# Optimization experiments

Measured on AMD Instinct MI355X. Metric: run time of the kernel, lower is better.

Reference implementation:

```python
import jax, jax.numpy as jnp
import numpy as np

# MX microscaling spec: block_size=32 shared power-of-2 scale, int8 elements (MXINT8),
# vector (SIMD) ops rounded to bfloat16 as in microxcaling's simd_* / vec_* ops.
BLOCK = 32
BITS = 8  # int8 element format: grid step 2^(shared_exp - (BITS-2)), range [-2^(BITS-1), 2^(BITS-1)-1]


def bf16_round(x):
    # bfloat=16 rounding used by simd_split / simd_add / vec ops
    return x.astype(jnp.bfloat16).astype(jnp.float32)


def mx_quant(x):
    """MXINT8 fake-quant along last (contraction) axis with block-shared exponent.
    Straight-through estimator for gradients."""
    s = x.shape
    xb = x.reshape(s[:-1] + (s[-1] // BLOCK, BLOCK))
    amax = jnp.max(jnp.abs(xb), axis=-1, keepdims=True)
    shared_exp = jnp.floor(jnp.log2(jnp.where(amax > 0, amax, 1.0)))
    scale = jnp.exp2(shared_exp - (BITS - 2))
    q = jnp.clip(jnp.round(xb / scale), -(2.0 ** (BITS - 1)), 2.0 ** (BITS - 1) - 1) * scale
    q = jnp.where(amax > 0, q, 0.0).reshape(s)
    return x + jax.lax.stop_gradient(q - x)


def mx_linear(x, W, b):
    # quantize activations and weights to MX blocks along K, fp32 accumulate, bf16 bias-add
    y = jnp.einsum('btk,ok->bto', mx_quant(x), mx_quant(W))
    return bf16_round(y + b)


def mx_layernorm(x, w, b, eps=1e-5):
    mu = jnp.mean(x, axis=-1, keepdims=True)
    var = jnp.mean(jnp.square(x - mu), axis=-1, keepdims=True)
    return bf16_round((x - mu) * jax.lax.rsqrt(var + eps) * w + b)


def mx_gelu(x):
    # tanh-approx gelu as in microxcaling, bf16-rounded output
    c = jnp.float32(0.7978845608028654)  # sqrt(2/pi)
    return bf16_round(0.5 * x * (1.0 + jnp.tanh(c * (x + 0.044715 * x * x * x))))


def setup_inputs() -> dict:
    key = jax.random.key(0)
    ks = jax.random.split(key, 5)
    B, S, H = 2, 2048, 2048
    inputs = jax.random.normal(ks[0], (B, S, H), dtype=jnp.float32)
    ln_w = jnp.ones((H,), dtype=jnp.float32)
    ln_b = jnp.zeros((H,), dtype=jnp.float32)
    W1 = jax.random.normal(ks[1], (4 * H, H), dtype=jnp.float32) * (1.0 / np.sqrt(H))
    b1 = jnp.zeros((4 * H,), dtype=jnp.float32)
    W2 = jax.random.normal(ks[2], (H, 4 * H), dtype=jnp.float32) * (1.0 / np.sqrt(4 * H))
    b2 = jnp.zeros((H,), dtype=jnp.float32)
    return {"inputs": inputs, "ln_w": ln_w, "ln_b": ln_b, "W1": W1, "b1": b1, "W2": W2, "b2": b2}


def reference(inputs, ln_w, ln_b, W1, b1, W2, b2):
    # simd_split: bf16-rounded copies for MLP branch and residual branch
    x = bf16_round(inputs)
    residual = bf16_round(inputs)
    h = mx_layernorm(x, ln_w, ln_b)
    h = mx_linear(h, W1, b1)          # [B,S,4H]
    h = mx_gelu(h)
    h = mx_linear(h, W2, b2)          # [B,S,H]
    return bf16_round(residual + h)    # simd_add
```

## Files before the change

kernel.cpp:

```cpp
#include <hip/hip_runtime.h>

#define DEVI __device__ __forceinline__

typedef __bf16 bf16x8 __attribute__((ext_vector_type(8)));
typedef float f32x4 __attribute__((ext_vector_type(4)));

DEVI unsigned short f2bf(float f) {
  unsigned u = __float_as_uint(f);
  u = (u + 0x7FFFu + ((u >> 16) & 1u)) >> 16;
  return (unsigned short)u;
}
DEVI float bf2f(unsigned short h) { return __uint_as_float(((unsigned)h) << 16); }
DEVI float bf16r(float f) { return bf2f(f2bf(f)); }

DEVI void mx_scales(float amax, float& scale, float& inv) {
  unsigned eb = __float_as_uint(amax) & 0x7f800000u;
  scale = __uint_as_float(eb - (6u << 23));
  inv   = __uint_as_float((260u << 23) - eb);
}

DEVI unsigned short quantv(float v, float scale, float inv) {
  float qv = rintf(v * inv);
  qv = fminf(fmaxf(qv, -128.f), 127.f);
  return f2bf(qv * scale);
}

DEVI void quant8(const float* h, float amax, unsigned short* q) {
  if (amax > 0.f) {
    float scale, inv;
    mx_scales(amax, scale, inv);
#pragma unroll
    for (int k = 0; k < 8; ++k) q[k] = quantv(h[k], scale, inv);
  } else {
#pragma unroll
    for (int k = 0; k < 8; ++k) q[k] = 0;
  }
}

template <int N>
DEVI float qmax_step(float x) {
  int y = __builtin_amdgcn_update_dpp(0, __float_as_int(x), 0x120 | N, 0xF, 0xF, true);
  return fmaxf(x, __int_as_float(y));
}
DEVI float quad_row_max(float x) {
  x = qmax_step<1>(x);
  x = qmax_step<2>(x);
  x = qmax_step<4>(x);
  x = qmax_step<8>(x);
  return x;
}

DEVI void gl2lds16(const void* g, void* l) {
  __builtin_amdgcn_global_load_lds(
      (__attribute__((address_space(1))) void*)const_cast<void*>(g),
      (__attribute__((address_space(3))) void*)l, 16, 0, 0);
}

DEVI uint4 pack8(const unsigned short* q) {
  uint4 o;
  o.x = (unsigned)q[0] | ((unsigned)q[1] << 16);
  o.y = (unsigned)q[2] | ((unsigned)q[3] << 16);
  o.z = (unsigned)q[4] | ((unsigned)q[5] << 16);
  o.w = (unsigned)q[6] | ((unsigned)q[7] << 16);
  return o;
}

__global__ __launch_bounds__(256) void prep_k(const float* __restrict__ W1,
                                              const float* __restrict__ W2,
                                              const float* __restrict__ X,
                                              const float* __restrict__ lw,
                                              const float* __restrict__ lb,
                                              unsigned short* __restrict__ qW1,
                                              unsigned short* __restrict__ qW2,
                                              unsigned short* __restrict__ a1) {
  __shared__ float red[4];
  const int bid = blockIdx.x;
  const int t = threadIdx.x;
  if (bid < 16384) {
    const float* src = (bid < 8192) ? W1 : W2;
    unsigned short* dst = (bid < 8192) ? qW1 : qW2;
    size_t idx = (size_t)(bid & 8191) * 256 + t;
    float4 v0 = ((const float4*)src)[idx * 2];
    float4 v1 = ((const float4*)src)[idx * 2 + 1];
    float h[8] = {v0.x, v0.y, v0.z, v0.w, v1.x, v1.y, v1.z, v1.w};
    float amax = 0.f;
#pragma unroll
    for (int k = 0; k < 8; ++k) amax = fmaxf(amax, fabsf(h[k]));
    amax = fmaxf(amax, __shfl_xor(amax, 1));
    amax = fmaxf(amax, __shfl_xor(amax, 2));
    unsigned short q[8];
    quant8(h, amax, q);
    ((uint4*)dst)[idx] = pack8(q);
  } else {
    const int H = 2048;
    const int row = bid - 16384;
    const int lane = t & 63, wave = t >> 6;
    const float* xr = X + (size_t)row * H;
    float4 v0 = ((const float4*)xr)[2 * t];
    float4 v1 = ((const float4*)xr)[2 * t + 1];
    float x[8] = {bf16r(v0.x), bf16r(v0.y), bf16r(v0.z), bf16r(v0.w),
                  bf16r(v1.x), bf16r(v1.y), bf16r(v1.z), bf16r(v1.w)};
    float s = 0.f;
#pragma unroll
    for (int k = 0; k < 8; ++k) s += x[k];
#pragma unroll
    for (int o = 32; o; o >>= 1) s += __shfl_xor(s, o);
    if (lane == 0) red[wave] = s;
    __syncthreads();
    float mu = (red[0] + red[1] + red[2] + red[3]) * (1.0f / H);
    __syncthreads();
    float v = 0.f;
#pragma unroll
    for (int k = 0; k < 8; ++k) { float d = x[k] - mu; v += d * d; }
#pragma unroll
    for (int o = 32; o; o >>= 1) v += __shfl_xor(v, o);
    if (lane == 0) red[wave] = v;
    __syncthreads();
    float var = (red[0] + red[1] + red[2] + red[3]) * (1.0f / H);
    float rstd = 1.0f / sqrtf(var + 1e-5f);
    float h[8];
    float amax = 0.f;
#pragma unroll
    for (int k = 0; k < 8; ++k) {
      int col = t * 8 + k;
      h[k] = bf16r((x[k] - mu) * rstd * lw[col] + lb[col]);
      amax = fmaxf(amax, fabsf(h[k]));
    }
    amax = fmaxf(amax, __shfl_xor(amax, 1));
    amax = fmaxf(amax, __shfl_xor(amax, 2));
    unsigned short q[8];
    quant8(h, amax, q);
    ((uint4*)(a1 + (size_t)row * H))[t] = pack8(q);
  }
}

template <int MODE>
__global__ __launch_bounds__(256) void gemm_mx(const unsigned short* __restrict__ A,
                                               const unsigned short* __restrict__ B,
                                               int M, int N, int K,
                                               const float* __restrict__ bias,
                                               const float* __restrict__ resid,
                                               void* __restrict__ outp) {
  __shared__ unsigned short As[128 * 64];
  __shared__ unsigned short Bs[128 * 64];

  const int tid = threadIdx.x;
  const int lane = tid & 63;
  const int wave = tid >> 6;
  const int wr = (wave >> 1) * 64;
  const int wc = (wave & 1) * 64;
  const int lr = lane & 15;
  const int quad = lane >> 4;

  const int m0 = blockIdx.y * 128;
  const int n0 = blockIdx.x * 128;

  size_t aoff[4], boff[4];
  int lbase[4];
#pragma unroll
  for (int j = 0; j < 4; ++j) {
    int n = j * 256 + tid;
    int r = n >> 3, c = (n & 7) ^ (r & 7);
    aoff[j] = (size_t)(m0 + r) * K + (size_t)c * 8;
    boff[j] = (size_t)(n0 + r) * K + (size_t)c * 8;
    lbase[j] = (j * 256 + (tid & ~63)) * 8;
  }

  f32x4 acc[4][4];
#pragma unroll
  for (int i = 0; i < 4; ++i)
#pragma unroll
    for (int j = 0; j < 4; ++j) acc[i][j] = (f32x4){0.f, 0.f, 0.f, 0.f};

  for (int k0 = 0; k0 < K; k0 += 64) {
#pragma unroll
    for (int j = 0; j < 4; ++j) gl2lds16(A + aoff[j] + k0, As + lbase[j]);
#pragma unroll
    for (int j = 0; j < 4; ++j) gl2lds16(B + boff[j] + k0, Bs + lbase[j]);
    __syncthreads();
#pragma unroll
    for (int s = 0; s < 2; ++s) {
      bf16x8 af[4], bfr[4];
#pragma unroll
      for (int i = 0; i < 4; ++i) {
        int row = wr + i * 16 + lr;
        int ch = (s * 4 + quad) ^ (row & 7);
        af[i] = *(const bf16x8*)(As + row * 64 + ch * 8);
      }
#pragma unroll
      for (int j = 0; j < 4; ++j) {
        int row = wc + j * 16 + lr;
        int ch = (s * 4 + quad) ^ (row & 7);
        bfr[j] = *(const bf16x8*)(Bs + row * 64 + ch * 8);
      }
#pragma unroll
      for (int i = 0; i < 4; ++i)
#pragma unroll
        for (int j = 0; j < 4; ++j)
          acc[i][j] = __builtin_amdgcn_mfma_f32_16x16x32_bf16(af[i], bfr[j], acc[i][j], 0, 0, 0);
    }
    __syncthreads();
  }

  if (MODE == 1) {
#pragma unroll
    for (int i = 0; i < 4; ++i) {
#pragma unroll
      for (int r = 0; r < 4; ++r) {
        const int gm = m0 + wr + i * 16 + quad * 4 + r;
        float g[4];
#pragma unroll
        for (int j = 0; j < 4; ++j) {
          float t = bf16r(acc[i][j][r] + bias[n0 + wc + j * 16 + lr]);
          float u = 0.7978845608028654f * (t + 0.044715f * t * t * t);
          g[j] = bf16r(0.5f * t * (1.0f + tanhf(u)));
        }
        float a = quad_row_max(fmaxf(fabsf(g[0]), fabsf(g[1])));
        float b = quad_row_max(fmaxf(fabsf(g[2]), fabsf(g[3])));
        unsigned short q[4];
        if (a > 0.f) {
          float sc, iv; mx_scales(a, sc, iv);
          q[0] = quantv(g[0], sc, iv); q[1] = quantv(g[1], sc, iv);
        } else { q[0] = q[1] = 0; }
        if (b > 0.f) {
          float sc, iv; mx_scales(b, sc, iv);
          q[2] = quantv(g[2], sc, iv); q[3] = quantv(g[3], sc, iv);
        } else { q[2] = q[3] = 0; }
        unsigned short* orow = (unsigned short*)outp + (size_t)gm * N + n0 + wc + lr;
#pragma unroll
        for (int j = 0; j < 4; ++j) orow[j * 16] = q[j];
      }
    }
  } else {
#pragma unroll
    for (int i = 0; i < 4; ++i) {
#pragma unroll
      for (int j = 0; j < 4; ++j) {
#pragma unroll
        for (int r = 0; r < 4; ++r) {
          int gm = m0 + wr + i * 16 + quad * 4 + r;
          int gn = n0 + wc + j * 16 + lr;
          float h = bf16r(acc[i][j][r] + bias[gn]);
          float rr = bf16r(resid[(size_t)gm * N + gn]);
          ((float*)outp)[(size_t)gm * N + gn] = bf16r(rr + h);
        }
      }
    }
  }
  (void)M;
}

extern "C" void kernel_launch(void* const* d_in, const int* in_sizes, int n_in,
                              void* d_out, int out_size, void* d_ws, size_t ws_size,
                              hipStream_t stream) {
  const float* inputs = (const float*)d_in[0];
  const float* ln_w   = (const float*)d_in[1];
  const float* ln_b   = (const float*)d_in[2];
  const float* W1     = (const float*)d_in[3];
  const float* b1     = (const float*)d_in[4];
  const float* W2     = (const float*)d_in[5];
  const float* b2     = (const float*)d_in[6];
  float* out = (float*)d_out;
  char* ws = (char*)d_ws;
  (void)in_sizes; (void)n_in; (void)out_size; (void)ws_size;

  unsigned short* qW1  = (unsigned short*)(ws);
  unsigned short* qW2  = (unsigned short*)(ws + (size_t)33554432);
  unsigned short* a1   = (unsigned short*)(ws + (size_t)67108864);
  unsigned short* act2 = (unsigned short*)(ws + (size_t)83886080);

  const int M = 4096;

  prep_k<<<20480, 256, 0, stream>>>(W1, W2, inputs, ln_w, ln_b, qW1, qW2, a1);

  gemm_mx<1><<<dim3(8192 / 128, M / 128), 256, 0, stream>>>(
      a1, qW1, M, 8192, 2048, b1, nullptr, (void*)act2);

  gemm_mx<2><<<dim3(2048 / 128, M / 128), 256, 0, stream>>>(
      act2, qW2, M, 2048, 8192, b2, inputs, (void*)out);
}
```

Baseline: 507.6 us.

## Triple-buffer GEMM LDS tiles with async prefetch and 128x256 block tiles

```diff
diff --git a/kernel.cpp b/kernel.cpp
--- a/kernel.cpp
+++ b/kernel.cpp
@@ -135,36 +135,38 @@
 }
 
 template <int MODE>
-__global__ __launch_bounds__(256) void gemm_mx(const unsigned short* __restrict__ A,
-                                               const unsigned short* __restrict__ B,
-                                               int M, int N, int K,
-                                               const float* __restrict__ bias,
-                                               const float* __restrict__ resid,
-                                               void* __restrict__ outp) {
-  __shared__ unsigned short As[128 * 64];
-  __shared__ unsigned short Bs[128 * 64];
+__global__ __launch_bounds__(512, 2) void gemm_mx(const unsigned short* __restrict__ A,
+                                                  const unsigned short* __restrict__ B,
+                                                  int M, int N, int K,
+                                                  const float* __restrict__ bias,
+                                                  const float* __restrict__ resid,
+                                                  void* __restrict__ outp) {
+  __shared__ __align__(16) unsigned short As[3][2][128 * 32];
+  __shared__ __align__(16) unsigned short Bs[3][2][256 * 32];
 
   const int tid = threadIdx.x;
   const int lane = tid & 63;
   const int wave = tid >> 6;
-  const int wr = (wave >> 1) * 64;
-  const int wc = (wave & 1) * 64;
   const int lr = lane & 15;
   const int quad = lane >> 4;
+  const int wr = (wave >> 2) * 64;
+  const int wc = (wave & 3) * 64;
 
   const int m0 = blockIdx.y * 128;
-  const int n0 = blockIdx.x * 128;
-
-  size_t aoff[4], boff[4];
-  int lbase[4];
-#pragma unroll
-  for (int j = 0; j < 4; ++j) {
-    int n = j * 256 + tid;
-    int r = n >> 3, c = (n & 7) ^ (r & 7);
-    aoff[j] = (size_t)(m0 + r) * K + (size_t)c * 8;
-    boff[j] = (size_t)(n0 + r) * K + (size_t)c * 8;
-    lbase[j] = (j * 256 + (tid & ~63)) * 8;
-  }
+  const int n0 = blockIdx.x * 256;
+
+  const int xsw = (quad ^ (lr & 3)) << 3;
+  const int lro = (wr + lr) * 32 + xsw;
+  const int lco = (wc + lr) * 32 + xsw;
+
+  const int sr = tid >> 2;
+  const int sc = ((tid & 3) ^ (sr & 3)) << 3;
+  const size_t aoff  = (size_t)(m0 + sr) * K + sc;
+  const size_t boff0 = (size_t)(n0 + sr) * K + sc;
+  const size_t boff1 = (size_t)(n0 + 128 + sr) * K + sc;
+  const int lbase = (tid & ~63) * 8;
+
+  const int NT = K >> 6;
 
   f32x4 acc[4][4];
 #pragma unroll
@@ -172,34 +174,54 @@
 #pragma unroll
     for (int j = 0; j < 4; ++j) acc[i][j] = (f32x4){0.f, 0.f, 0.f, 0.f};
 
-  for (int k0 = 0; k0 < K; k0 += 64) {
-#pragma unroll
-    for (int j = 0; j < 4; ++j) gl2lds16(A + aoff[j] + k0, As + lbase[j]);
-#pragma unroll
-    for (int j = 0; j < 4; ++j) gl2lds16(B + boff[j] + k0, Bs + lbase[j]);
-    __syncthreads();
+#pragma unroll
+  for (int pt = 0; pt < 2; ++pt)
+#pragma unroll
+    for (int s = 0; s < 2; ++s) {
+      const size_t kadd = (size_t)pt * 64 + s * 32;
+      gl2lds16(A + aoff + kadd, &As[pt][s][lbase]);
+      gl2lds16(B + boff0 + kadd, &Bs[pt][s][lbase]);
+      gl2lds16(B + boff1 + kadd, &Bs[pt][s][4096 + lbase]);
+    }
+  asm volatile("s_waitcnt vmcnt(6)" ::: "memory");
+  __builtin_amdgcn_s_barrier();
+
+  int buf = 0;
+  for (int t = 0; t < NT; ++t) {
+    int nbuf = buf + 2; if (nbuf >= 3) nbuf -= 3;
+    const bool pf = (t + 2) < NT;
 #pragma unroll
     for (int s = 0; s < 2; ++s) {
       bf16x8 af[4], bfr[4];
-#pragma unroll
-      for (int i = 0; i < 4; ++i) {
-        int row = wr + i * 16 + lr;
-        int ch = (s * 4 + quad) ^ (row & 7);
-        af[i] = *(const bf16x8*)(As + row * 64 + ch * 8);
+      const unsigned short* Ap = &As[buf][s][0];
+      const unsigned short* Bp = &Bs[buf][s][0];
+#pragma unroll
+      for (int i = 0; i < 4; ++i) af[i] = *(const bf16x8*)(Ap + lro + i * 512);
+#pragma unroll
+      for (int j = 0; j < 4; ++j) bfr[j] = *(const bf16x8*)(Bp + lco + j * 512);
+      if (pf) {
+        const size_t kadd = (size_t)(t + 2) * 64 + s * 32;
+        gl2lds16(A + aoff + kadd, &As[nbuf][s][lbase]);
+        gl2lds16(B + boff0 + kadd, &Bs[nbuf][s][lbase]);
+        gl2lds16(B + boff1 + kadd, &Bs[nbuf][s][4096 + lbase]);
       }
-#pragma unroll
-      for (int j = 0; j < 4; ++j) {
-        int row = wc + j * 16 + lr;
-        int ch = (s * 4 + quad) ^ (row & 7);
-        bfr[j] = *(const bf16x8*)(Bs + row * 64 + ch * 8);
-      }
+      __builtin_amdgcn_s_barrier();
+      asm volatile("s_waitcnt lgkmcnt(0)" ::: "memory");
+      __builtin_amdgcn_sched_barrier(0);
+      __builtin_amdgcn_s_setprio(1);
 #pragma unroll
       for (int i = 0; i < 4; ++i)
 #pragma unroll
         for (int j = 0; j < 4; ++j)
           acc[i][j] = __builtin_amdgcn_mfma_f32_16x16x32_bf16(af[i], bfr[j], acc[i][j], 0, 0, 0);
-    }
-    __syncthreads();
+      __builtin_amdgcn_s_setprio(0);
+      if (s == 1) {
+        if (pf) asm volatile("s_waitcnt vmcnt(6)" ::: "memory");
+        else    asm volatile("s_waitcnt vmcnt(0)" ::: "memory");
+      }
+      __builtin_amdgcn_s_barrier();
+    }
+    if (++buf == 3) buf = 0;
   }
 
   if (MODE == 1) {
@@ -211,20 +233,20 @@
         float g[4];
 #pragma unroll
         for (int j = 0; j < 4; ++j) {
-          float t = bf16r(acc[i][j][r] + bias[n0 + wc + j * 16 + lr]);
-          float u = 0.7978845608028654f * (t + 0.044715f * t * t * t);
-          g[j] = bf16r(0.5f * t * (1.0f + tanhf(u)));
+          float tt = bf16r(acc[i][j][r] + bias[n0 + wc + j * 16 + lr]);
+          float u = 0.7978845608028654f * (tt + 0.044715f * tt * tt * tt);
+          g[j] = bf16r(0.5f * tt * (1.0f + tanhf(u)));
         }
         float a = quad_row_max(fmaxf(fabsf(g[0]), fabsf(g[1])));
         float b = quad_row_max(fmaxf(fabsf(g[2]), fabsf(g[3])));
         unsigned short q[4];
         if (a > 0.f) {
-          float sc, iv; mx_scales(a, sc, iv);
-          q[0] = quantv(g[0], sc, iv); q[1] = quantv(g[1], sc, iv);
+          float sc2, iv; mx_scales(a, sc2, iv);
+          q[0] = quantv(g[0], sc2, iv); q[1] = quantv(g[1], sc2, iv);
         } else { q[0] = q[1] = 0; }
         if (b > 0.f) {
-          float sc, iv; mx_scales(b, sc, iv);
-          q[2] = quantv(g[2], sc, iv); q[3] = quantv(g[3], sc, iv);
+          float sc2, iv; mx_scales(b, sc2, iv);
+          q[2] = quantv(g[2], sc2, iv); q[3] = quantv(g[3], sc2, iv);
         } else { q[2] = q[3] = 0; }
         unsigned short* orow = (unsigned short*)outp + (size_t)gm * N + n0 + wc + lr;
 #pragma unroll
@@ -273,9 +295,9 @@
 
   prep_k<<<20480, 256, 0, stream>>>(W1, W2, inputs, ln_w, ln_b, qW1, qW2, a1);
 
-  gemm_mx<1><<<dim3(8192 / 128, M / 128), 256, 0, stream>>>(
+  gemm_mx<1><<<dim3(8192 / 256, M / 128), 512, 0, stream>>>(
       a1, qW1, M, 8192, 2048, b1, nullptr, (void*)act2);
 
-  gemm_mx<2><<<dim3(2048 / 128, M / 128), 256, 0, stream>>>(
+  gemm_mx<2><<<dim3(2048 / 256, M / 128), 512, 0, stream>>>(
       act2, qW2, M, 2048, 8192, b2, inputs, (void*)out);
 }
```

After: 558.4 us. 10.0% more time.

## Rewrite both GEMMs with multi-stage LDS pipelining, larger tiles and swizzled block order

Applied to the files above, without the earlier changes.

```diff
diff --git a/kernel.cpp b/kernel.cpp
--- a/kernel.cpp
+++ b/kernel.cpp
@@ -4,6 +4,9 @@
 
 typedef __bf16 bf16x8 __attribute__((ext_vector_type(8)));
 typedef float f32x4 __attribute__((ext_vector_type(4)));
+
+#define WAIT_VM(n) asm volatile("s_waitcnt vmcnt(" #n ")" ::: "memory")
+#define WAIT_LGKM(n) asm volatile("s_waitcnt lgkmcnt(" #n ")" ::: "memory")
 
 DEVI unsigned short f2bf(float f) {
   unsigned u = __float_as_uint(f);
@@ -134,37 +137,166 @@
   }
 }
 
-template <int MODE>
-__global__ __launch_bounds__(256) void gemm_mx(const unsigned short* __restrict__ A,
-                                               const unsigned short* __restrict__ B,
-                                               int M, int N, int K,
-                                               const float* __restrict__ bias,
-                                               const float* __restrict__ resid,
-                                               void* __restrict__ outp) {
-  __shared__ unsigned short As[128 * 64];
-  __shared__ unsigned short Bs[128 * 64];
+__global__ __launch_bounds__(512, 2) void gemm1_k(const unsigned short* __restrict__ A,
+                                                  const unsigned short* __restrict__ B,
+                                                  const float* __restrict__ bias,
+                                                  unsigned short* __restrict__ outp) {
+  constexpr int K = 2048, N = 8192, NT = K / 32;
+  __shared__ __align__(16) unsigned short As[4 * 8192];
+  __shared__ __align__(16) unsigned short Bs[4 * 8192];
 
   const int tid = threadIdx.x;
   const int lane = tid & 63;
-  const int wave = tid >> 6;
-  const int wr = (wave >> 1) * 64;
-  const int wc = (wave & 1) * 64;
   const int lr = lane & 15;
   const int quad = lane >> 4;
-
-  const int m0 = blockIdx.y * 128;
-  const int n0 = blockIdx.x * 128;
-
-  size_t aoff[4], boff[4];
-  int lbase[4];
-#pragma unroll
-  for (int j = 0; j < 4; ++j) {
-    int n = j * 256 + tid;
-    int r = n >> 3, c = (n & 7) ^ (r & 7);
-    aoff[j] = (size_t)(m0 + r) * K + (size_t)c * 8;
-    boff[j] = (size_t)(n0 + r) * K + (size_t)c * 8;
-    lbase[j] = (j * 256 + (tid & ~63)) * 8;
-  }
+  const int wave = tid >> 6;
+  const int wm = wave >> 2;
+  const int wn = wave & 3;
+
+  int lin = blockIdx.y * 32 + blockIdx.x;
+  lin = (lin & 7) * 64 + (lin >> 3);
+  const int m0 = (lin >> 5) * 256;
+  const int n0 = (lin & 31) * 256;
+
+  const int chq = quad ^ ((lr >> 1) & 3);
+  const int aro = (wm * 128 + lr) * 32 + chq * 8;
+  const int bro = (wn * 64 + lr) * 32 + chq * 8;
+
+  const int srow = tid >> 2;
+  const int sch = (tid & 3) ^ ((tid >> 3) & 3);
+  const size_t aoff = (size_t)(m0 + srow) * K + sch * 8;
+  const size_t boff = (size_t)(n0 + srow) * K + sch * 8;
+  const int lb = (tid & ~63) * 8;
+
+  f32x4 acc[8][4];
+#pragma unroll
+  for (int i = 0; i < 8; ++i)
+#pragma unroll
+    for (int j = 0; j < 4; ++j) acc[i][j] = (f32x4){0.f, 0.f, 0.f, 0.f};
+
+  bf16x8 af0[4], af1[4], bA[4], bB[4];
+
+#define G1_STAGE_A(T) { int bf_ = (T) & 3;                                         \
+    gl2lds16(A + aoff + (size_t)(T) * 32, As + bf_ * 8192 + lb);                   \
+    gl2lds16(A + aoff + (size_t)128 * K + (size_t)(T) * 32, As + bf_ * 8192 + 4096 + lb); }
+#define G1_STAGE_B(T) { int bf_ = (T) & 3;                                         \
+    gl2lds16(B + boff + (size_t)(T) * 32, Bs + bf_ * 8192 + lb);                   \
+    gl2lds16(B + boff + (size_t)128 * K + (size_t)(T) * 32, Bs + bf_ * 8192 + 4096 + lb); }
+
+#pragma unroll
+  for (int pt = 0; pt < 3; ++pt) { G1_STAGE_A(pt); G1_STAGE_B(pt); }
+  WAIT_VM(8);
+  __builtin_amdgcn_s_barrier();
+#pragma unroll
+  for (int i = 0; i < 4; ++i) af0[i] = *(const bf16x8*)(As + aro + i * 512);
+#pragma unroll
+  for (int j = 0; j < 4; ++j) bA[j] = *(const bf16x8*)(Bs + bro + j * 512);
+
+#define G1_TILE(T, BC, BN_) {                                                      \
+    const unsigned short* Ab_ = As + ((T) & 3) * 8192;                             \
+    const bool pf3 = (T) + 3 < NT, pf2 = (T) + 2 < NT, pf1 = (T) + 1 < NT;         \
+                      \
+    if (pf3) G1_STAGE_A((T) + 3);                                                  \
+    _Pragma("unroll")                                                              \
+    for (int i = 0; i < 4; ++i) af1[i] = *(const bf16x8*)(Ab_ + aro + 2048 + i * 512); \
+    if (pf3) { WAIT_VM(6); } else if (pf2) { WAIT_VM(4); } else { WAIT_VM(0); }    \
+    WAIT_LGKM(4);                                                                  \
+    __builtin_amdgcn_sched_barrier(0);                                             \
+    __builtin_amdgcn_s_setprio(1);                                                 \
+    _Pragma("unroll")                                                              \
+    for (int i = 0; i < 4; ++i)                                                    \
+      _Pragma("unroll")                                                            \
+      for (int j = 0; j < 4; ++j)                                                  \
+        acc[i][j] = __builtin_amdgcn_mfma_f32_16x16x32_bf16(af0[i], BC[j], acc[i][j], 0, 0, 0); \
+    __builtin_amdgcn_s_setprio(0);                                                 \
+    __builtin_amdgcn_s_barrier();                                                  \
+           \
+    if (pf3) G1_STAGE_B((T) + 3);                                                  \
+    if (pf1) {                                                                     \
+      const unsigned short* An_ = As + (((T) + 1) & 3) * 8192;                     \
+      const unsigned short* Bn_ = Bs + (((T) + 1) & 3) * 8192;                     \
+      _Pragma("unroll")                                                            \
+      for (int i = 0; i < 4; ++i) af0[i] = *(const bf16x8*)(An_ + aro + i * 512);  \
+      _Pragma("unroll")                                                            \
+      for (int j = 0; j < 4; ++j) BN_[j] = *(const bf16x8*)(Bn_ + bro + j * 512);  \
+      WAIT_LGKM(8);                                                                \
+    } else { WAIT_LGKM(0); }                                                       \
+    __builtin_amdgcn_sched_barrier(0);                                             \
+    __builtin_amdgcn_s_setprio(1);                                                 \
+    _Pragma("unroll")                                                              \
+    for (int i = 0; i < 4; ++i)                                                    \
+      _Pragma("unroll")                                                            \
+      for (int j = 0; j < 4; ++j)                                                  \
+        acc[4 + i][j] = __builtin_amdgcn_mfma_f32_16x16x32_bf16(af1[i], BC[j], acc[4 + i][j], 0, 0, 0); \
+    __builtin_amdgcn_s_setprio(0);                                                 \
+    __builtin_amdgcn_s_barrier(); }
+
+  for (int t = 0; t < NT; t += 2) {
+    G1_TILE(t, bA, bB);
+    G1_TILE(t + 1, bB, bA);
+  }
+
+#pragma unroll
+  for (int i = 0; i < 8; ++i) {
+#pragma unroll
+    for (int r = 0; r < 4; ++r) {
+      const int gm = m0 + wm * 128 + i * 16 + quad * 4 + r;
+      float g[4];
+#pragma unroll
+      for (int j = 0; j < 4; ++j) {
+        float tt = bf16r(acc[i][j][r] + bias[n0 + wn * 64 + j * 16 + lr]);
+        float u = 0.7978845608028654f * (tt + 0.044715f * tt * tt * tt);
+        g[j] = bf16r(0.5f * tt * (1.0f + tanhf(u)));
+      }
+      float a = quad_row_max(fmaxf(fabsf(g[0]), fabsf(g[1])));
+      float b = quad_row_max(fmaxf(fabsf(g[2]), fabsf(g[3])));
+      unsigned short q[4];
+      if (a > 0.f) {
+        float sc2, iv; mx_scales(a, sc2, iv);
+        q[0] = quantv(g[0], sc2, iv); q[1] = quantv(g[1], sc2, iv);
+      } else { q[0] = q[1] = 0; }
+      if (b > 0.f) {
+        float sc2, iv; mx_scales(b, sc2, iv);
+        q[2] = quantv(g[2], sc2, iv); q[3] = quantv(g[3], sc2, iv);
+      } else { q[2] = q[3] = 0; }
+      unsigned short* orow = outp + (size_t)gm * N + n0 + wn * 64 + lr;
+#pragma unroll
+      for (int j = 0; j < 4; ++j) orow[j * 16] = q[j];
+    }
+  }
+}
+
+__global__ __launch_bounds__(512, 2) void gemm2_k(const unsigned short* __restrict__ A,
+                                                  const unsigned short* __restrict__ B,
+                                                  const float* __restrict__ bias,
+                                                  const float* __restrict__ resid,
+                                                  float* __restrict__ outp) {
+  constexpr int K = 8192, N = 2048, NT = K / 32;
+  __shared__ __align__(16) unsigned short As[5 * 4096];
+  __shared__ __align__(16) unsigned short Bs[5 * 8192];
+
+  const int tid = threadIdx.x;
+  const int lane = tid & 63;
+  const int lr = lane & 15;
+  const int quad = lane >> 4;
+  const int wave = tid >> 6;
+  const int wm = wave >> 2;
+  const int wn = wave & 3;
+
+  int lin = blockIdx.y * 8 + blockIdx.x;
+  lin = (lin & 7) * 32 + (lin >> 3);
+  const int m0 = (lin >> 3) * 128;
+  const int n0 = (lin & 7) * 256;
+
+  const int chq = quad ^ ((lr >> 1) & 3);
+  const int aro = (wm * 64 + lr) * 32 + chq * 8;
+  const int bro = (wn * 64 + lr) * 32 + chq * 8;
+
+  const int srow = tid >> 2;
+  const int sch = (tid & 3) ^ ((tid >> 3) & 3);
+  const size_t aoff = (size_t)(m0 + srow) * K + sch * 8;
+  const size_t boff = (size_t)(n0 + srow) * K + sch * 8;
+  const int lb = (tid & ~63) * 8;
 
   f32x4 acc[4][4];
 #pragma unroll
@@ -172,82 +304,64 @@
 #pragma unroll
     for (int j = 0; j < 4; ++j) acc[i][j] = (f32x4){0.f, 0.f, 0.f, 0.f};
 
-  for (int k0 = 0; k0 < K; k0 += 64) {
-#pragma unroll
-    for (int j = 0; j < 4; ++j) gl2lds16(A + aoff[j] + k0, As + lbase[j]);
-#pragma unroll
-    for (int j = 0; j < 4; ++j) gl2lds16(B + boff[j] + k0, Bs + lbase[j]);
-    __syncthreads();
-#pragma unroll
-    for (int s = 0; s < 2; ++s) {
-      bf16x8 af[4], bfr[4];
-#pragma unroll
-      for (int i = 0; i < 4; ++i) {
-        int row = wr + i * 16 + lr;
-        int ch = (s * 4 + quad) ^ (row & 7);
-        af[i] = *(const bf16x8*)(As + row * 64 + ch * 8);
-      }
-#pragma unroll
-      for (int j = 0; j < 4; ++j) {
-        int row = wc + j * 16 + lr;
-        int ch = (s * 4 + quad) ^ (row & 7);
-        bfr[j] = *(const bf16x8*)(Bs + row * 64 + ch * 8);
-      }
-#pragma unroll
-      for (int i = 0; i < 4; ++i)
-#pragma unroll
-        for (int j = 0; j < 4; ++j)
-          acc[i][j] = __builtin_amdgcn_mfma_f32_16x16x32_bf16(af[i], bfr[j], acc[i][j], 0, 0, 0);
-    }
-    __syncthreads();
-  }
-
-  if (MODE == 1) {
-#pragma unroll
-    for (int i = 0; i < 4; ++i) {
+  bf16x8 afX[4], bX[4], afY[4], bY[4];
+
+#define G2_STAGE(T) { int bf_ = (T) % 5;                                           \
+    gl2lds16(A + aoff + (size_t)(T) * 32, As + bf_ * 4096 + lb);                   \
+    gl2lds16(B + boff + (size_t)(T) * 32, Bs + bf_ * 8192 + lb);                   \
+    gl2lds16(B + boff + (size_t)128 * K + (size_t)(T) * 32, Bs + bf_ * 8192 + 4096 + lb); }
+
+#pragma unroll
+  for (int pt = 0; pt < 4; ++pt) G2_STAGE(pt);
+  WAIT_VM(6);
+  __builtin_amdgcn_s_barrier();
+#pragma unroll
+  for (int i = 0; i < 4; ++i) afX[i] = *(const bf16x8*)(As + aro + i * 512);
+#pragma unroll
+  for (int j = 0; j < 4; ++j) bX[j] = *(const bf16x8*)(Bs + bro + j * 512);
+
+#define G2_TILE(T, AC, BC, AN, BN_) {                                              \
+    const bool pf4 = (T) + 4 < NT, pf3 = (T) + 3 < NT, pf1 = (T) + 1 < NT;         \
+    if (pf1) {                                                                     \
+      const unsigned short* An_ = As + (((T) + 1) % 5) * 4096;                     \
+      const unsigned short* Bn_ = Bs + (((T) + 1) % 5) * 8192;                     \
+      _Pragma("unroll")                                                            \
+      for (int i = 0; i < 4; ++i) AN[i] = *(const bf16x8*)(An_ + aro + i * 512);   \
+      _Pragma("unroll")                                                            \
+      for (int j = 0; j < 4; ++j) BN_[j] = *(const bf16x8*)(Bn_ + bro + j * 512);  \
+    }                                                                              \
+    if (pf4) G2_STAGE((T) + 4);                                                    \
+    if (pf4) { WAIT_VM(6); } else if (pf3) { WAIT_VM(3); } else { WAIT_VM(0); }    \
+    if (pf1) { WAIT_LGKM(8); } else { WAIT_LGKM(0); }                              \
+    __builtin_amdgcn_sched_barrier(0);                                             \
+    __builtin_amdgcn_s_setprio(1);                                                 \
+    _Pragma("unroll")                                                              \
+    for (int i = 0; i < 4; ++i)                                                    \
+      _Pragma("unroll")                                                            \
+      for (int j = 0; j < 4; ++j)                                                  \
+        acc[i][j] = __builtin_amdgcn_mfma_f32_16x16x32_bf16(AC[i], BC[j], acc[i][j], 0, 0, 0); \
+    __builtin_amdgcn_s_setprio(0);                                                 \
+    __builtin_amdgcn_s_barrier(); }
+
+  for (int t = 0; t < NT; t += 2) {
+    G2_TILE(t, afX, bX, afY, bY);
+    G2_TILE(t + 1, afY, bY, afX, bX);
+  }
+
+#pragma unroll
+  for (int i = 0; i < 4; ++i) {
+#pragma unroll
+    for (int j = 0; j < 4; ++j) {
 #pragma unroll
       for (int r = 0; r < 4; ++r) {
-        const int gm = m0 + wr + i * 16 + quad * 4 + r;
-        float g[4];
-#pragma unroll
-        for (int j = 0; j < 4; ++j) {
-          float t = bf16r(acc[i][j][r] + bias[n0 + wc + j * 16 + lr]);
-          float u = 0.7978845608028654f * (t + 0.044715f * t * t * t);
-          g[j] = bf16r(0.5f * t * (1.0f + tanhf(u)));
-        }
-        float a = quad_row_max(fmaxf(fabsf(g[0]), fabsf(g[1])));
-        float b = quad_row_max(fmaxf(fabsf(g[2]), fabsf(g[3])));
-        unsigned short q[4];
-        if (a > 0.f) {
-          float sc, iv; mx_scales(a, sc, iv);
-          q[0] = quantv(g[0], sc, iv); q[1] = quantv(g[1], sc, iv);
-        } else { q[0] = q[1] = 0; }
-        if (b > 0.f) {
-          float sc, iv; mx_scales(b, sc, iv);
-          q[2] = quantv(g[2], sc, iv); q[3] = quantv(g[3], sc, iv);
-        } else { q[2] = q[3] = 0; }
-        unsigned short* orow = (unsigned short*)outp + (size_t)gm * N + n0 + wc + lr;
-#pragma unroll
-        for (int j = 0; j < 4; ++j) orow[j * 16] = q[j];
+        int gm = m0 + wm * 64 + i * 16 + quad * 4 + r;
+        int gn = n0 + wn * 64 + j * 16 + lr;
+        float h = bf16r(acc[i][j][r] + bias[gn]);
+        float rr = bf16r(resid[(size_t)gm * N + gn]);
+        outp[(size_t)gm * N + gn] = bf16r(rr + h);
       }
     }
-  } else {
-#pragma unroll
-    for (int i = 0; i < 4; ++i) {
-#pragma unroll
-      for (int j = 0; j < 4; ++j) {
-#pragma unroll
-        for (int r = 0; r < 4; ++r) {
-          int gm = m0 + wr + i * 16 + quad * 4 + r;
-          int gn = n0 + wc + j * 16 + lr;
-          float h = bf16r(acc[i][j][r] + bias[gn]);
-          float rr = bf16r(resid[(size_t)gm * N + gn]);
-          ((float*)outp)[(size_t)gm * N + gn] = bf16r(rr + h);
-        }
-      }
-    }
-  }
-  (void)M;
+  }
 }
 
 extern "C" void kernel_launch(void* const* d_in, const int* in_sizes, int n_in,
@@ -269,13 +383,9 @@
   unsigned short* a1   = (unsigned short*)(ws + (size_t)67108864);
   unsigned short* act2 = (unsigned short*)(ws + (size_t)83886080);
 
-  const int M = 4096;
-
   prep_k<<<20480, 256, 0, stream>>>(W1, W2, inputs, ln_w, ln_b, qW1, qW2, a1);
 
-  gemm_mx<1><<<dim3(8192 / 128, M / 128), 256, 0, stream>>>(
-      a1, qW1, M, 8192, 2048, b1, nullptr, (void*)act2);
-
-  gemm_mx<2><<<dim3(2048 / 128, M / 128), 256, 0, stream>>>(
-      act2, qW2, M, 2048, 8192, b2, inputs, (void*)out);
-}
+  gemm1_k<<<dim3(8192 / 256, 4096 / 256), 512, 0, stream>>>(a1, qW1, b1, act2);
+
+  gemm2_k<<<dim3(2048 / 256, 4096 / 128), 512, 0, stream>>>(act2, qW2, b2, inputs, out);
+}
```

After: 538.5 us. 6.1% more time.

## Load B fragments directly from global into registers with double-buffered prefetch

Applied to the files above, without the earlier changes.

```diff
diff --git a/kernel.cpp b/kernel.cpp
--- a/kernel.cpp
+++ b/kernel.cpp
@@ -142,7 +142,6 @@
                                                const float* __restrict__ resid,
                                                void* __restrict__ outp) {
   __shared__ unsigned short As[128 * 64];
-  __shared__ unsigned short Bs[128 * 64];
 
   const int tid = threadIdx.x;
   const int lane = tid & 63;
@@ -155,52 +154,76 @@
   const int m0 = blockIdx.y * 128;
   const int n0 = blockIdx.x * 128;
 
-  size_t aoff[4], boff[4];
+  size_t aoff[4];
   int lbase[4];
 #pragma unroll
   for (int j = 0; j < 4; ++j) {
     int n = j * 256 + tid;
     int r = n >> 3, c = (n & 7) ^ (r & 7);
     aoff[j] = (size_t)(m0 + r) * K + (size_t)c * 8;
-    boff[j] = (size_t)(n0 + r) * K + (size_t)c * 8;
     lbase[j] = (j * 256 + (tid & ~63)) * 8;
   }
 
+  int arow[4];
+#pragma unroll
+  for (int i = 0; i < 4; ++i) arow[i] = (wr + i * 16 + lr) * 64;
+  const int ch0 = (quad ^ (lr & 7)) * 8;
+  const int ch1 = ((4 + quad) ^ (lr & 7)) * 8;
+
+  const unsigned short* bbase = B + (size_t)(n0 + wc + lr) * K + quad * 8;
+  const int brstep = 16 * K;
+
   f32x4 acc[4][4];
 #pragma unroll
   for (int i = 0; i < 4; ++i)
 #pragma unroll
     for (int j = 0; j < 4; ++j) acc[i][j] = (f32x4){0.f, 0.f, 0.f, 0.f};
 
-  for (int k0 = 0; k0 < K; k0 += 64) {
-#pragma unroll
-    for (int j = 0; j < 4; ++j) gl2lds16(A + aoff[j] + k0, As + lbase[j]);
-#pragma unroll
-    for (int j = 0; j < 4; ++j) gl2lds16(B + boff[j] + k0, Bs + lbase[j]);
-    __syncthreads();
-#pragma unroll
-    for (int s = 0; s < 2; ++s) {
-      bf16x8 af[4], bfr[4];
-#pragma unroll
-      for (int i = 0; i < 4; ++i) {
-        int row = wr + i * 16 + lr;
-        int ch = (s * 4 + quad) ^ (row & 7);
-        af[i] = *(const bf16x8*)(As + row * 64 + ch * 8);
-      }
-#pragma unroll
-      for (int j = 0; j < 4; ++j) {
-        int row = wc + j * 16 + lr;
-        int ch = (s * 4 + quad) ^ (row & 7);
-        bfr[j] = *(const bf16x8*)(Bs + row * 64 + ch * 8);
-      }
-#pragma unroll
-      for (int i = 0; i < 4; ++i)
-#pragma unroll
-        for (int j = 0; j < 4; ++j)
-          acc[i][j] = __builtin_amdgcn_mfma_f32_16x16x32_bf16(af[i], bfr[j], acc[i][j], 0, 0, 0);
-    }
-    __syncthreads();
-  }
+  const int NT = K >> 6;
+
+  bf16x8 bX0[4], bX1[4], bY0[4], bY1[4];
+#pragma unroll
+  for (int j = 0; j < 4; ++j) {
+    bX0[j] = *(const bf16x8*)(bbase + j * brstep);
+    bX1[j] = *(const bf16x8*)(bbase + j * brstep + 32);
+  }
+
+#define G_TILE(T, BC0, BC1, BN0, BN1)                                           \
+  {                                                                             \
+    const int k0_ = (T) * 64;                                                   \
+    _Pragma("unroll")                                                           \
+    for (int j = 0; j < 4; ++j) gl2lds16(A + aoff[j] + k0_, As + lbase[j]);     \
+    __syncthreads();                                          \
+    if ((T) + 1 < NT) {          \
+      _Pragma("unroll")                                                         \
+      for (int j = 0; j < 4; ++j) {                                             \
+        BN0[j] = *(const bf16x8*)(bbase + j * brstep + k0_ + 64);               \
+        BN1[j] = *(const bf16x8*)(bbase + j * brstep + k0_ + 96);               \
+      }                                                                         \
+    }                                                                           \
+    bf16x8 af[4];                                                               \
+    _Pragma("unroll")                                                           \
+    for (int i = 0; i < 4; ++i) af[i] = *(const bf16x8*)(As + arow[i] + ch0);   \
+    _Pragma("unroll")                                                           \
+    for (int i = 0; i < 4; ++i)                                                 \
+      _Pragma("unroll")                                                         \
+      for (int j = 0; j < 4; ++j)                                               \
+        acc[i][j] = __builtin_amdgcn_mfma_f32_16x16x32_bf16(af[i], BC0[j], acc[i][j], 0, 0, 0); \
+    _Pragma("unroll")                                                           \
+    for (int i = 0; i < 4; ++i) af[i] = *(const bf16x8*)(As + arow[i] + ch1);   \
+    _Pragma("unroll")                                                           \
+    for (int i = 0; i < 4; ++i)                                                 \
+      _Pragma("unroll")                                                         \
+      for (int j = 0; j < 4; ++j)                                               \
+        acc[i][j] = __builtin_amdgcn_mfma_f32_16x16x32_bf16(af[i], BC1[j], acc[i][j], 0, 0, 0); \
+    __syncthreads();     \
+  }
+
+  for (int t = 0; t < NT; t += 2) {
+    G_TILE(t, bX0, bX1, bY0, bY1);
+    G_TILE(t + 1, bY0, bY1, bX0, bX1);
+  }
+#undef G_TILE
 
   if (MODE == 1) {
 #pragma unroll
```

After: 758.6 us. +49.4%, slower.
